# Kernel optimization log

Hardware: AMD Instinct MI355X
Metric: run time of the kernel (lower is better)

The kernel has to match this reference:

```python
import jax, jax.numpy as jnp
import numpy as np

EPS = 1e-5  # BatchNorm eps (torch default)


def point_sample(feat, points):
    """Bilinear sample feat [B,C,Hf,Wf] at points [B,K,2] (x,y in [0,1]),
    matching F.grid_sample(2*p-1, mode='bilinear', padding_mode='zeros',
    align_corners=False)."""
    B, C, Hf, Wf = feat.shape
    x = points[..., 0] * Wf - 0.5  # [B,K] pixel coords
    y = points[..., 1] * Hf - 0.5
    x0f = jnp.floor(x); y0f = jnp.floor(y)
    wx = (x - x0f)[:, None, :]  # [B,1,K]
    wy = (y - y0f)[:, None, :]
    x0 = x0f.astype(jnp.int32); y0 = y0f.astype(jnp.int32)
    flat = feat.reshape(B, C, Hf * Wf)

    def gather(xi, yi):
        valid = ((xi >= 0) & (xi < Wf) & (yi >= 0) & (yi < Hf))[:, None, :]
        lin = jnp.clip(yi, 0, Hf - 1) * Wf + jnp.clip(xi, 0, Wf - 1)  # [B,K]
        idx = jnp.broadcast_to(lin[:, None, :], (B, C, lin.shape[1]))
        return jnp.take_along_axis(flat, idx, axis=2) * valid

    v00 = gather(x0, y0)
    v10 = gather(x0 + 1, y0)
    v01 = gather(x0, y0 + 1)
    v11 = gather(x0 + 1, y0 + 1)
    return (v00 * (1 - wx) * (1 - wy) + v10 * wx * (1 - wy)
            + v01 * (1 - wx) * wy + v11 * wx * wy)


def bn(x, g, b, m, v):
    # eval-mode BatchNorm1d over channel dim of [B,C,K]
    scale = (g / jnp.sqrt(v + EPS))[None, :, None]
    return (x - m[None, :, None]) * scale + b[None, :, None]


def setup_inputs() -> dict:
    key = jax.random.key(0)
    ks = jax.random.split(key, 20)
    B, H, W = 8, 512, 512
    Cf = 256
    d = {
        'uncertainty_map': jax.random.normal(ks[0], (B, 1, H, W), jnp.float32),
        'prev_mask': jax.random.uniform(ks[1], (B, 1, H, W), jnp.float32),
        'enc_f': jax.random.normal(ks[2], (B, Cf, 128, 128), jnp.float32),
        'w1': jax.random.normal(ks[3], (256, Cf + 1), jnp.float32) * 0.05,
        'b1': jax.random.normal(ks[4], (256,), jnp.float32) * 0.05,
        'g1': jnp.ones((256,), jnp.float32),
        'be1': jnp.zeros((256,), jnp.float32),
        'm1': jax.random.normal(ks[5], (256,), jnp.float32) * 0.1,
        'v1': jax.random.uniform(ks[6], (256,), jnp.float32) + 0.5,
        'w2': jax.random.normal(ks[7], (256, 256), jnp.float32) * 0.05,
        'b2': jax.random.normal(ks[8], (256,), jnp.float32) * 0.05,
        'g2': jnp.ones((256,), jnp.float32),
        'be2': jnp.zeros((256,), jnp.float32),
        'm2': jax.random.normal(ks[9], (256,), jnp.float32) * 0.1,
        'v2': jax.random.uniform(ks[10], (256,), jnp.float32) + 0.5,
        'w3': jax.random.normal(ks[11], (1, 256), jnp.float32) * 0.05,
        'b3': jax.random.normal(ks[12], (1,), jnp.float32) * 0.05,
    }
    return d


def reference(uncertainty_map, prev_mask, enc_f,
              w1, b1, g1, be1, m1, v1,
              w2, b2, g2, be2, m2, v2,
              w3, b3):
    B, C, H, W = prev_mask.shape
    K = H * W // 10
    # K least-uncertain points (topk largest=False)
    _, idx = jax.lax.top_k(-uncertainty_map.reshape(B, -1), K)  # [B,K] int32
    col = (idx % W).astype(jnp.float32)
    row = (idx // W).astype(jnp.float32)
    points = jnp.stack([(col + 0.5) / W, (row + 0.5) / H], axis=-1)  # [B,K,2]

    coarse = point_sample(prev_mask, points)  # [B,1,K]
    fine = point_sample(enc_f, points)        # [B,Cf,K]
    h = jnp.concatenate([coarse, fine], axis=1)  # [B,Cf+1,K]

    h = jax.nn.relu(bn(jnp.einsum('oc,bck->bok', w1, h) + b1[None, :, None], g1, be1, m1, v1))
    h = jax.nn.relu(bn(jnp.einsum('oc,bck->bok', w2, h) + b2[None, :, None], g2, be2, m2, v2))
    refined = jax.nn.sigmoid(jnp.einsum('oc,bck->bok', w3, h) + b3[None, :, None])  # [B,1,K]

    flat = prev_mask.reshape(B, C, H * W)
    bi = jnp.arange(B)[:, None, None]
    ci = jnp.arange(C)[None, :, None]
    out = flat.at[bi, ci, idx[:, None, :]].set(jnp.broadcast_to(refined, (B, C, K)))
    return out.reshape(B, C, H, W)
```

## Files before the change

### kernel.cpp

```cpp
#include <hip/hip_runtime.h>
#include <hip/hip_bf16.h>

#define HW_IMG 262144
#define KSEL   26214
#define NB     8
#define CF     256
#define LDW1   288
#define LDACT  296

typedef short    short8 __attribute__((ext_vector_type(8)));
typedef float    f32x4  __attribute__((ext_vector_type(4)));
typedef unsigned u32x2  __attribute__((ext_vector_type(2)));
typedef unsigned short u16x4 __attribute__((ext_vector_type(4)));

__device__ __forceinline__ unsigned f2key(float f){
    unsigned u = __builtin_bit_cast(unsigned, f);
    return (u & 0x80000000u) ? ~u : (u | 0x80000000u);
}
__device__ __forceinline__ unsigned short f2bf(float f){
    unsigned u = __builtin_bit_cast(unsigned, f);
    u = u + 0x7FFFu + ((u >> 16) & 1u);
    return (unsigned short)(u >> 16);
}
__device__ __forceinline__ float bf2f(unsigned short s){
    unsigned u = ((unsigned)s) << 16;
    return __builtin_bit_cast(float, u);
}

__global__ __launch_bounds__(256) void k_prep(
    const float* __restrict__ w1, const float* __restrict__ w2,
    const float* __restrict__ b1, const float* __restrict__ g1, const float* __restrict__ be1,
    const float* __restrict__ m1, const float* __restrict__ v1,
    const float* __restrict__ b2, const float* __restrict__ g2, const float* __restrict__ be2,
    const float* __restrict__ m2, const float* __restrict__ v2,
    unsigned short* __restrict__ w1p, unsigned short* __restrict__ w2p,
    float* __restrict__ c1, float* __restrict__ c2)
{
    int tid = blockIdx.x * 256 + threadIdx.x;
    if (tid < 256 * LDW1) {
        int o = tid / LDW1, k = tid % LDW1;
        float scale = g1[o] * rsqrtf(v1[o] + 1e-5f);
        float val = 0.f;
        if (k < 256) val = w1[o * 257 + k + 1];
        else if (k == 256) val = w1[o * 257];
        w1p[tid] = f2bf(val * scale);
        if (k == 0) c1[o] = (b1[o] - m1[o]) * scale + be1[o];
    } else {
        int t2 = tid - 256 * LDW1;
        if (t2 < 65536) {
            int o = t2 >> 8;
            float scale = g2[o] * rsqrtf(v2[o] + 1e-5f);
            w2p[t2] = f2bf(w2[t2] * scale);
            if ((t2 & 255) == 0) c2[o] = (b2[o] - m2[o]) * scale + be2[o];
        }
    }
}

__global__ __launch_bounds__(256) void k_transpose(
    const float* __restrict__ enc, unsigned short* __restrict__ encT)
{
    __shared__ __align__(16) unsigned short tile[64][72];
    int b = blockIdx.z;
    int pixbase = blockIdx.x * 64;
    int chbase  = blockIdx.y * 64;
    int t = threadIdx.x;
    int pix = t & 63, cg = t >> 6;
    const float* src = enc + (size_t)b * CF * 16384;
#pragma unroll
    for (int i = 0; i < 16; i++) {
        int c = chbase + cg * 16 + i;
        tile[pix][cg * 16 + i] = f2bf(src[(size_t)c * 16384 + pixbase + pix]);
    }
    __syncthreads();
    unsigned short* dst = encT + (size_t)b * 16384 * CF;
#pragma unroll
    for (int pass = 0; pass < 4; pass++) {
        int pl = pass * 16 + (t >> 4);
        int c4 = (t & 15) * 4;
        *(u16x4*)(dst + (size_t)(pixbase + pl) * CF + chbase + c4) = *(const u16x4*)&tile[pl][c4];
    }
}


__global__ __launch_bounds__(256) void k_histA(const float* __restrict__ unc, unsigned* __restrict__ hist)
{
    __shared__ unsigned lh[4][4096];
    int b = blockIdx.y, t = threadIdx.x;
    int wv = t >> 6;
    for (int i = t; i < 4 * 4096; i += 256) ((unsigned*)lh)[i] = 0;
    __syncthreads();
    const float4* src = (const float4*)(unc + (size_t)b * HW_IMG + blockIdx.x * 4096);
    unsigned* mine = lh[wv];
#pragma unroll
    for (int j = 0; j < 4; j++) {
        float4 v = src[j * 256 + t];
        atomicAdd(&mine[f2key(v.x) >> 20], 1u);
        atomicAdd(&mine[f2key(v.y) >> 20], 1u);
        atomicAdd(&mine[f2key(v.z) >> 20], 1u);
        atomicAdd(&mine[f2key(v.w) >> 20], 1u);
    }
    __syncthreads();
    unsigned* gh = hist + (size_t)b * 4096;
    for (int i = t; i < 4096; i += 256) {
        unsigned c = lh[0][i] + lh[1][i] + lh[2][i] + lh[3][i];
        if (c) atomicAdd(&gh[i], c);
    }
}

__global__ __launch_bounds__(256) void k_histB(const float* __restrict__ unc,
    const unsigned* __restrict__ meta, unsigned* __restrict__ hist)
{
    __shared__ unsigned lh[4096];
    int b = blockIdx.y, t = threadIdx.x;
    unsigned binA = meta[b * 8 + 0];
    for (int i = t; i < 4096; i += 256) lh[i] = 0;
    __syncthreads();
    const float4* src = (const float4*)(unc + (size_t)b * HW_IMG + blockIdx.x * 4096);
#pragma unroll
    for (int j = 0; j < 4; j++) {
        float4 v = src[j * 256 + t];
        unsigned k;
        k = f2key(v.x); if ((k >> 20) == binA) atomicAdd(&lh[(k >> 8) & 0xFFFu], 1u);
        k = f2key(v.y); if ((k >> 20) == binA) atomicAdd(&lh[(k >> 8) & 0xFFFu], 1u);
        k = f2key(v.z); if ((k >> 20) == binA) atomicAdd(&lh[(k >> 8) & 0xFFFu], 1u);
        k = f2key(v.w); if ((k >> 20) == binA) atomicAdd(&lh[(k >> 8) & 0xFFFu], 1u);
    }
    __syncthreads();
    unsigned* gh = hist + (size_t)b * 4096;
    for (int i = t; i < 4096; i += 256) { unsigned c = lh[i]; if (c) atomicAdd(&gh[i], c); }
}

__global__ __launch_bounds__(256) void k_histC(const float* __restrict__ unc,
    const unsigned* __restrict__ meta, unsigned* __restrict__ hist)
{
    __shared__ unsigned lh[256];
    int b = blockIdx.y, t = threadIdx.x;
    unsigned pre24 = (meta[b * 8 + 0] << 12) | meta[b * 8 + 2];
    lh[t] = 0;
    __syncthreads();
    const float4* src = (const float4*)(unc + (size_t)b * HW_IMG + blockIdx.x * 4096);
#pragma unroll
    for (int j = 0; j < 4; j++) {
        float4 v = src[j * 256 + t];
        unsigned k;
        k = f2key(v.x); if ((k >> 8) == pre24) atomicAdd(&lh[k & 0xFFu], 1u);
        k = f2key(v.y); if ((k >> 8) == pre24) atomicAdd(&lh[k & 0xFFu], 1u);
        k = f2key(v.z); if ((k >> 8) == pre24) atomicAdd(&lh[k & 0xFFu], 1u);
        k = f2key(v.w); if ((k >> 8) == pre24) atomicAdd(&lh[k & 0xFFu], 1u);
    }
    __syncthreads();
    unsigned* gh = hist + (size_t)b * 4096;
    unsigned c = lh[t];
    if (c) atomicAdd(&gh[t], c);
}

__global__ __launch_bounds__(256) void k_find(const unsigned* __restrict__ hist,
    unsigned* __restrict__ meta, int per, int stage)
{
    int b = blockIdx.x, t = threadIdx.x;
    const unsigned* h = hist + (size_t)b * 4096;
    unsigned base = (stage == 0) ? 0u : meta[b * 8 + 2 * stage - 1];
    __shared__ unsigned seg[256], pref[256];
    unsigned s = 0;
    for (int i = 0; i < per; i++) s += h[t * per + i];
    seg[t] = s;
    __syncthreads();
    if (t == 0) { unsigned c = base; for (int i = 0; i < 256; i++) { pref[i] = c; c += seg[i]; } }
    __syncthreads();
    if (pref[t] < KSEL && KSEL <= pref[t] + seg[t]) {
        unsigned c = pref[t];
        for (int i = 0; i < per; i++) {
            unsigned cnt = h[t * per + i];
            if (c + cnt >= KSEL) {
                unsigned bin = (unsigned)(t * per + i);
                meta[b * 8 + 2 * stage] = bin;
                meta[b * 8 + 2 * stage + 1] = c;
                if (stage == 2)
                    meta[b * 8 + 6] = (meta[b * 8 + 0] << 20) | (meta[b * 8 + 2] << 8) | bin;
                break;
            }
            c += cnt;
        }
    }
}

__global__ __launch_bounds__(256) void k_count(const float* __restrict__ unc,
    const unsigned* __restrict__ meta, unsigned* __restrict__ cntL, unsigned* __restrict__ cntE)
{
    int b = blockIdx.y, blk = blockIdx.x, t = threadIdx.x;
    unsigned pivot = meta[b * 8 + 6];
    const float4* src = (const float4*)(unc + (size_t)b * HW_IMG + blk * 1024);
    float4 v = src[t];
    unsigned k0 = f2key(v.x), k1 = f2key(v.y), k2 = f2key(v.z), k3 = f2key(v.w);
    unsigned cl = (k0 < pivot) + (k1 < pivot) + (k2 < pivot) + (k3 < pivot);
    unsigned ce = (k0 == pivot) + (k1 == pivot) + (k2 == pivot) + (k3 == pivot);
    __shared__ unsigned rl[256], re[256];
    rl[t] = cl; re[t] = ce; __syncthreads();
    for (int s = 128; s > 0; s >>= 1) { if (t < s) { rl[t] += rl[t + s]; re[t] += re[t + s]; } __syncthreads(); }
    if (t == 0) { cntL[b * 256 + blk] = rl[0]; cntE[b * 256 + blk] = re[0]; }
}

__global__ void k_scan(const unsigned* __restrict__ cntL, const unsigned* __restrict__ cntE,
                       unsigned* __restrict__ offL, unsigned* __restrict__ offE)
{
    int b = blockIdx.x;
    if (threadIdx.x == 0) {
        unsigned c = 0;
        for (int i = 0; i < 256; i++) { offL[b * 256 + i] = c; c += cntL[b * 256 + i]; }
        c = 0;
        for (int i = 0; i < 256; i++) { offE[b * 256 + i] = c; c += cntE[b * 256 + i]; }
    }
}

__global__ __launch_bounds__(256) void k_emit(const float* __restrict__ unc,
    const unsigned* __restrict__ meta, const unsigned* __restrict__ offL,
    const unsigned* __restrict__ offE, unsigned* __restrict__ sel)
{
    int b = blockIdx.y, blk = blockIdx.x, t = threadIdx.x;
    unsigned pivot = meta[b * 8 + 6], cless = meta[b * 8 + 5], r = KSEL - cless;
    int base = blk * 1024 + t * 4;
    const float4* src = (const float4*)(unc + (size_t)b * HW_IMG + blk * 1024);
    float4 v = src[t];
    unsigned key[4] = { f2key(v.x), f2key(v.y), f2key(v.z), f2key(v.w) };
    unsigned cl = 0, ce = 0;
#pragma unroll
    for (int j = 0; j < 4; j++) { cl += (key[j] < pivot); ce += (key[j] == pivot); }
    __shared__ unsigned sL[256], sE[256];
    sL[t] = cl; sE[t] = ce; __syncthreads();
    for (int off = 1; off < 256; off <<= 1) {
        unsigned aL = (t >= off) ? sL[t - off] : 0u;
        unsigned aE = (t >= off) ? sE[t - off] : 0u;
        __syncthreads();
        sL[t] += aL; sE[t] += aE;
        __syncthreads();
    }
    unsigned posL = offL[b * 256 + blk] + sL[t] - cl;
    unsigned posE = offE[b * 256 + blk] + sE[t] - ce;
    unsigned* sb = sel + (size_t)b * KSEL;
#pragma unroll
    for (int j = 0; j < 4; j++) {
        if (key[j] < pivot) { sb[posL++] = (unsigned)(base + j); }
        else if (key[j] == pivot) { if (posE < r) sb[cless + posE] = (unsigned)(base + j); posE++; }
    }
}

__global__ __launch_bounds__(256, 2) void k_main(
    const unsigned* __restrict__ sel, const float* __restrict__ prev,
    const unsigned short* __restrict__ encT,
    const unsigned short* __restrict__ w1p, const unsigned short* __restrict__ w2p,
    const float* __restrict__ c1, const float* __restrict__ c2,
    const float* __restrict__ w3, const float* __restrict__ b3,
    float* __restrict__ out)
{
    __shared__ __align__(16) unsigned short act[64][LDACT];
    __shared__ unsigned sIdx[64];
    __shared__ float sPart[4][64];

    int b = blockIdx.y;
    int pbase = blockIdx.x * 64;
    int npts = KSEL - pbase; if (npts > 64) npts = 64;
    int t = threadIdx.x;

    if (t < 64) {
        unsigned id = (t < npts) ? sel[(size_t)b * KSEL + pbase + t] : 0u;
        sIdx[t] = id;
        act[t][256] = f2bf(prev[(size_t)b * HW_IMG + id]);
#pragma unroll
        for (int k = 257; k < LDW1; k++) act[t][k] = 0;
    }
    __syncthreads();

    {
        int wv = t >> 6, l = t & 63;
        int g = l >> 2, sub = l & 3;
        int p = wv * 16 + g;
        unsigned id = sIdx[p];
        int col = id & 511, row = (int)(id >> 9);
        float xf = (col - 1.5f) * 0.25f;
        float yf = (row - 1.5f) * 0.25f;
        float x0f = floorf(xf), y0f = floorf(yf);
        int x0 = (int)x0f, y0 = (int)y0f;
        float wx = xf - x0f, wy = yf - y0f;
        float wxa = (x0 >= 0) ? (1.f - wx) : 0.f;
        float wxb = (x0 <= 126) ? wx : 0.f;
        float wya = (y0 >= 0) ? (1.f - wy) : 0.f;
        float wyb = (y0 <= 126) ? wy : 0.f;
        int xc0 = x0 < 0 ? 0 : x0;
        int xc1 = (x0 + 1 > 127) ? 127 : x0 + 1;
        int yc0 = y0 < 0 ? 0 : y0;
        int yc1 = (y0 + 1 > 127) ? 127 : y0 + 1;
        float w00 = wxa * wya, w10 = wxb * wya, w01 = wxa * wyb, w11 = wxb * wyb;
        const unsigned short* bb = encT + (size_t)b * 16384 * CF + sub * 64;
        const unsigned short* p00 = bb + (size_t)(yc0 * 128 + xc0) * CF;
        const unsigned short* p10 = bb + (size_t)(yc0 * 128 + xc1) * CF;
        const unsigned short* p01 = bb + (size_t)(yc1 * 128 + xc0) * CF;
        const unsigned short* p11 = bb + (size_t)(yc1 * 128 + xc1) * CF;
#pragma unroll 2
        for (int ch = 0; ch < 8; ch++) {
            short8 va = *(const short8*)(p00 + ch * 8);
            short8 vb = *(const short8*)(p10 + ch * 8);
            short8 vc = *(const short8*)(p01 + ch * 8);
            short8 vd = *(const short8*)(p11 + ch * 8);
            short8 rr;
#pragma unroll
            for (int j = 0; j < 8; j++) {
                float f = w00 * bf2f((unsigned short)va[j]) + w10 * bf2f((unsigned short)vb[j])
                        + w01 * bf2f((unsigned short)vc[j]) + w11 * bf2f((unsigned short)vd[j]);
                rr[j] = (short)f2bf(f);
            }
            *(short8*)&act[p][sub * 64 + ch * 8] = rr;
        }
    }
    __syncthreads();

    int wv = t >> 6, l = t & 63;
    int lr = l & 15, lk = l >> 4;
    f32x4 acc[4][4];
#pragma unroll
    for (int m = 0; m < 4; m++)
#pragma unroll
        for (int n = 0; n < 4; n++) acc[m][n] = (f32x4){0.f, 0.f, 0.f, 0.f};

#pragma unroll
    for (int kk = 0; kk < 9; kk++) {
        int k0 = kk * 32 + lk * 8;
        short8 afr[4], bfr[4];
#pragma unroll
        for (int m = 0; m < 4; m++)
            afr[m] = *(const short8*)(w1p + (size_t)(wv * 64 + m * 16 + lr) * LDW1 + k0);
#pragma unroll
        for (int n = 0; n < 4; n++)
            bfr[n] = *(const short8*)&act[n * 16 + lr][k0];
#pragma unroll
        for (int m = 0; m < 4; m++)
#pragma unroll
            for (int n = 0; n < 4; n++)
                acc[m][n] = __builtin_amdgcn_mfma_f32_16x16x32_bf16(afr[m], bfr[n], acc[m][n], 0, 0, 0);
    }
    __syncthreads();

#pragma unroll
    for (int m = 0; m < 4; m++) {
        int chb = wv * 64 + m * 16 + lk * 4;
        float c0 = c1[chb], cA = c1[chb + 1], cB = c1[chb + 2], cC = c1[chb + 3];
#pragma unroll
        for (int n = 0; n < 4; n++) {
            int p = n * 16 + lr;
            float v0 = fmaxf(acc[m][n][0] + c0, 0.f);
            float v1 = fmaxf(acc[m][n][1] + cA, 0.f);
            float v2 = fmaxf(acc[m][n][2] + cB, 0.f);
            float v3 = fmaxf(acc[m][n][3] + cC, 0.f);
            u32x2 pk;
            pk[0] = (unsigned)f2bf(v0) | ((unsigned)f2bf(v1) << 16);
            pk[1] = (unsigned)f2bf(v2) | ((unsigned)f2bf(v3) << 16);
            *(u32x2*)&act[p][chb] = pk;
        }
    }
    __syncthreads();

#pragma unroll
    for (int m = 0; m < 4; m++)
#pragma unroll
        for (int n = 0; n < 4; n++) acc[m][n] = (f32x4){0.f, 0.f, 0.f, 0.f};
#pragma unroll
    for (int kk = 0; kk < 8; kk++) {
        int k0 = kk * 32 + lk * 8;
        short8 afr[4], bfr[4];
#pragma unroll
        for (int m = 0; m < 4; m++)
            afr[m] = *(const short8*)(w2p + (size_t)(wv * 64 + m * 16 + lr) * 256 + k0);
#pragma unroll
        for (int n = 0; n < 4; n++)
            bfr[n] = *(const short8*)&act[n * 16 + lr][k0];
#pragma unroll
        for (int m = 0; m < 4; m++)
#pragma unroll
            for (int n = 0; n < 4; n++)
                acc[m][n] = __builtin_amdgcn_mfma_f32_16x16x32_bf16(afr[m], bfr[n], acc[m][n], 0, 0, 0);
    }

    float part[4] = {0.f, 0.f, 0.f, 0.f};
#pragma unroll
    for (int m = 0; m < 4; m++) {
        int chb = wv * 64 + m * 16 + lk * 4;
#pragma unroll
        for (int r = 0; r < 4; r++) {
            float wr = w3[chb + r];
            float cr = c2[chb + r];
#pragma unroll
            for (int n = 0; n < 4; n++)
                part[n] += wr * fmaxf(acc[m][n][r] + cr, 0.f);
        }
    }
#pragma unroll
    for (int n = 0; n < 4; n++) {
        part[n] += __shfl_xor(part[n], 16);
        part[n] += __shfl_xor(part[n], 32);
    }
    if (lk == 0) {
#pragma unroll
        for (int n = 0; n < 4; n++) sPart[wv][n * 16 + lr] = part[n];
    }
    __syncthreads();
    if (t < 64) {
        float tot = sPart[0][t] + sPart[1][t] + sPart[2][t] + sPart[3][t] + b3[0];
        float refined = 1.f / (1.f + __expf(-tot));
        if (t < npts) out[(size_t)b * HW_IMG + sIdx[t]] = refined;
    }
}

extern "C" void kernel_launch(void* const* d_in, const int* in_sizes, int n_in,
                              void* d_out, int out_size, void* d_ws, size_t ws_size,
                              hipStream_t stream)
{
    (void)in_sizes; (void)n_in; (void)out_size; (void)ws_size;
    const float* unc  = (const float*)d_in[0];
    const float* prev = (const float*)d_in[1];
    const float* enc  = (const float*)d_in[2];
    const float* w1   = (const float*)d_in[3];
    const float* b1   = (const float*)d_in[4];
    const float* g1   = (const float*)d_in[5];
    const float* be1  = (const float*)d_in[6];
    const float* m1   = (const float*)d_in[7];
    const float* v1   = (const float*)d_in[8];
    const float* w2   = (const float*)d_in[9];
    const float* b2   = (const float*)d_in[10];
    const float* g2   = (const float*)d_in[11];
    const float* be2  = (const float*)d_in[12];
    const float* m2   = (const float*)d_in[13];
    const float* v2   = (const float*)d_in[14];
    const float* w3   = (const float*)d_in[15];
    const float* b3   = (const float*)d_in[16];
    float* out = (float*)d_out;

    char* ws = (char*)d_ws;
    size_t off = 0;
    auto alloc = [&](size_t bytes) { size_t o = off; off += (bytes + 255) & ~(size_t)255; return o; };
    size_t o_encT = alloc((size_t)NB * 16384 * CF * 2);
    size_t o_w1p  = alloc((size_t)256 * LDW1 * 2);
    size_t o_w2p  = alloc((size_t)256 * 256 * 2);
    size_t o_c1   = alloc(256 * 4);
    size_t o_c2   = alloc(256 * 4);
    size_t o_hist = alloc((size_t)3 * NB * 4096 * 4);
    size_t o_meta = alloc(NB * 8 * 4);
    size_t o_cntL = alloc(NB * 256 * 4);
    size_t o_cntE = alloc(NB * 256 * 4);
    size_t o_offL = alloc(NB * 256 * 4);
    size_t o_offE = alloc(NB * 256 * 4);
    size_t o_sel  = alloc((size_t)NB * KSEL * 4);

    unsigned short* encT = (unsigned short*)(ws + o_encT);
    unsigned short* w1p  = (unsigned short*)(ws + o_w1p);
    unsigned short* w2p  = (unsigned short*)(ws + o_w2p);
    float* c1p = (float*)(ws + o_c1);
    float* c2p = (float*)(ws + o_c2);
    unsigned* histA = (unsigned*)(ws + o_hist);
    unsigned* histB = histA + (size_t)NB * 4096;
    unsigned* histC = histB + (size_t)NB * 4096;
    unsigned* meta  = (unsigned*)(ws + o_meta);
    unsigned* cntL  = (unsigned*)(ws + o_cntL);
    unsigned* cntE  = (unsigned*)(ws + o_cntE);
    unsigned* offL  = (unsigned*)(ws + o_offL);
    unsigned* offE  = (unsigned*)(ws + o_offE);
    unsigned* sel   = (unsigned*)(ws + o_sel);

    hipMemsetAsync(ws + o_hist, 0, (size_t)3 * NB * 4096 * 4, stream);
    hipMemcpyAsync(d_out, (const void*)prev, (size_t)NB * HW_IMG * 4, hipMemcpyDeviceToDevice, stream);

    k_prep<<<544, 256, 0, stream>>>(w1, w2, b1, g1, be1, m1, v1, b2, g2, be2, m2, v2,
                                    w1p, w2p, c1p, c2p);
    k_transpose<<<dim3(256, 4, NB), 256, 0, stream>>>(enc, encT);

    k_histA<<<dim3(64, NB), 256, 0, stream>>>(unc, histA);
    k_find <<<NB, 256, 0, stream>>>(histA, meta, 16, 0);
    k_histB<<<dim3(64, NB), 256, 0, stream>>>(unc, meta, histB);
    k_find <<<NB, 256, 0, stream>>>(histB, meta, 16, 1);
    k_histC<<<dim3(64, NB), 256, 0, stream>>>(unc, meta, histC);
    k_find <<<NB, 256, 0, stream>>>(histC, meta, 1, 2);
    k_count<<<dim3(256, NB), 256, 0, stream>>>(unc, meta, cntL, cntE);
    k_scan <<<NB, 64, 0, stream>>>(cntL, cntE, offL, offE);
    k_emit <<<dim3(256, NB), 256, 0, stream>>>(unc, meta, offL, offE, sel);

    k_main<<<dim3((KSEL + 63) / 64, NB), 256, 0, stream>>>(sel, prev, encT, w1p, w2p,
                                                           c1p, c2p, w3, b3, out);
}
```

Baseline: 244.8 us.

## Fuse find/scan stages into histogram kernels via last-block pattern and swizzle activation LDS

Removes the separate k_find and k_scan launches by having the last finishing block per batch (found with an atomic done counter) run the threshold search or a parallel prefix scan. This cuts kernel launches and serial single-thread scans. The main kernel also gets an XOR-swizzled activation layout in shared memory to reduce bank conflicts, a higher occupancy target, a flattened batch-interleaved grid, deeper unrolling of the gather loop, and no shared-memory index staging. The risks are extra atomics and fences, and possible register spills under the tighter launch bounds.

```diff
diff --git a/kernel.cpp b/kernel.cpp
--- a/kernel.cpp
+++ b/kernel.cpp
@@ -7,6 +7,9 @@
 #define CF     256
 #define LDW1   288
 #define LDACT  296
+#define NBLK_MAIN 410
+
+#define ACOL(c) ((c) ^ ((((c) >> 6) & 3) << 4))
 
 typedef short    short8 __attribute__((ext_vector_type(8)));
 typedef float    f32x4  __attribute__((ext_vector_type(4)));
@@ -82,90 +85,18 @@
 }
 
 
-__global__ __launch_bounds__(256) void k_histA(const float* __restrict__ unc, unsigned* __restrict__ hist)
-{
-    __shared__ unsigned lh[4][4096];
-    int b = blockIdx.y, t = threadIdx.x;
-    int wv = t >> 6;
-    for (int i = t; i < 4 * 4096; i += 256) ((unsigned*)lh)[i] = 0;
-    __syncthreads();
-    const float4* src = (const float4*)(unc + (size_t)b * HW_IMG + blockIdx.x * 4096);
-    unsigned* mine = lh[wv];
-#pragma unroll
-    for (int j = 0; j < 4; j++) {
-        float4 v = src[j * 256 + t];
-        atomicAdd(&mine[f2key(v.x) >> 20], 1u);
-        atomicAdd(&mine[f2key(v.y) >> 20], 1u);
-        atomicAdd(&mine[f2key(v.z) >> 20], 1u);
-        atomicAdd(&mine[f2key(v.w) >> 20], 1u);
-    }
-    __syncthreads();
-    unsigned* gh = hist + (size_t)b * 4096;
-    for (int i = t; i < 4096; i += 256) {
-        unsigned c = lh[0][i] + lh[1][i] + lh[2][i] + lh[3][i];
-        if (c) atomicAdd(&gh[i], c);
-    }
-}
-
-__global__ __launch_bounds__(256) void k_histB(const float* __restrict__ unc,
-    const unsigned* __restrict__ meta, unsigned* __restrict__ hist)
-{
-    __shared__ unsigned lh[4096];
-    int b = blockIdx.y, t = threadIdx.x;
-    unsigned binA = meta[b * 8 + 0];
-    for (int i = t; i < 4096; i += 256) lh[i] = 0;
-    __syncthreads();
-    const float4* src = (const float4*)(unc + (size_t)b * HW_IMG + blockIdx.x * 4096);
-#pragma unroll
-    for (int j = 0; j < 4; j++) {
-        float4 v = src[j * 256 + t];
-        unsigned k;
-        k = f2key(v.x); if ((k >> 20) == binA) atomicAdd(&lh[(k >> 8) & 0xFFFu], 1u);
-        k = f2key(v.y); if ((k >> 20) == binA) atomicAdd(&lh[(k >> 8) & 0xFFFu], 1u);
-        k = f2key(v.z); if ((k >> 20) == binA) atomicAdd(&lh[(k >> 8) & 0xFFFu], 1u);
-        k = f2key(v.w); if ((k >> 20) == binA) atomicAdd(&lh[(k >> 8) & 0xFFFu], 1u);
-    }
-    __syncthreads();
-    unsigned* gh = hist + (size_t)b * 4096;
-    for (int i = t; i < 4096; i += 256) { unsigned c = lh[i]; if (c) atomicAdd(&gh[i], c); }
-}
-
-__global__ __launch_bounds__(256) void k_histC(const float* __restrict__ unc,
-    const unsigned* __restrict__ meta, unsigned* __restrict__ hist)
-{
-    __shared__ unsigned lh[256];
-    int b = blockIdx.y, t = threadIdx.x;
-    unsigned pre24 = (meta[b * 8 + 0] << 12) | meta[b * 8 + 2];
-    lh[t] = 0;
-    __syncthreads();
-    const float4* src = (const float4*)(unc + (size_t)b * HW_IMG + blockIdx.x * 4096);
-#pragma unroll
-    for (int j = 0; j < 4; j++) {
-        float4 v = src[j * 256 + t];
-        unsigned k;
-        k = f2key(v.x); if ((k >> 8) == pre24) atomicAdd(&lh[k & 0xFFu], 1u);
-        k = f2key(v.y); if ((k >> 8) == pre24) atomicAdd(&lh[k & 0xFFu], 1u);
-        k = f2key(v.z); if ((k >> 8) == pre24) atomicAdd(&lh[k & 0xFFu], 1u);
-        k = f2key(v.w); if ((k >> 8) == pre24) atomicAdd(&lh[k & 0xFFu], 1u);
-    }
-    __syncthreads();
-    unsigned* gh = hist + (size_t)b * 4096;
-    unsigned c = lh[t];
-    if (c) atomicAdd(&gh[t], c);
-}
-
-__global__ __launch_bounds__(256) void k_find(const unsigned* __restrict__ hist,
-    unsigned* __restrict__ meta, int per, int stage)
-{
-    int b = blockIdx.x, t = threadIdx.x;
-    const unsigned* h = hist + (size_t)b * 4096;
-    unsigned base = (stage == 0) ? 0u : meta[b * 8 + 2 * stage - 1];
+__device__ __forceinline__ void find_stage(const unsigned* __restrict__ h,
+    unsigned* __restrict__ meta, int b, int per, int stage, int t)
+{
     __shared__ unsigned seg[256], pref[256];
     unsigned s = 0;
     for (int i = 0; i < per; i++) s += h[t * per + i];
     seg[t] = s;
     __syncthreads();
-    if (t == 0) { unsigned c = base; for (int i = 0; i < 256; i++) { pref[i] = c; c += seg[i]; } }
+    if (t == 0) {
+        unsigned c = (stage == 0) ? 0u : meta[b * 8 + 2 * stage - 1];
+        for (int i = 0; i < 256; i++) { pref[i] = c; c += seg[i]; }
+    }
     __syncthreads();
     if (pref[t] < KSEL && KSEL <= pref[t] + seg[t]) {
         unsigned c = pref[t];
@@ -184,8 +115,98 @@
     }
 }
 
+__device__ __forceinline__ bool last_block(unsigned* done, int b, int nblk, int t)
+{
+    __shared__ unsigned sT;
+    __threadfence();
+    __syncthreads();
+    if (t == 0) sT = atomicAdd(&done[b], 1u);
+    __syncthreads();
+    if (sT == (unsigned)(nblk - 1)) { __threadfence(); return true; }
+    return false;
+}
+
+__global__ __launch_bounds__(256) void k_histA(const float* __restrict__ unc,
+    unsigned* __restrict__ hist, unsigned* __restrict__ meta, unsigned* __restrict__ done)
+{
+    __shared__ unsigned lh[4][4096];
+    int b = blockIdx.y, t = threadIdx.x;
+    int wv = t >> 6;
+    for (int i = t; i < 4 * 4096; i += 256) ((unsigned*)lh)[i] = 0;
+    __syncthreads();
+    const float4* src = (const float4*)(unc + (size_t)b * HW_IMG + blockIdx.x * 4096);
+    unsigned* mine = lh[wv];
+#pragma unroll
+    for (int j = 0; j < 4; j++) {
+        float4 v = src[j * 256 + t];
+        atomicAdd(&mine[f2key(v.x) >> 20], 1u);
+        atomicAdd(&mine[f2key(v.y) >> 20], 1u);
+        atomicAdd(&mine[f2key(v.z) >> 20], 1u);
+        atomicAdd(&mine[f2key(v.w) >> 20], 1u);
+    }
+    __syncthreads();
+    unsigned* gh = hist + (size_t)b * 4096;
+    for (int i = t; i < 4096; i += 256) {
+        unsigned c = lh[0][i] + lh[1][i] + lh[2][i] + lh[3][i];
+        if (c) atomicAdd(&gh[i], c);
+    }
+    if (last_block(done, b, gridDim.x, t)) find_stage(gh, meta, b, 16, 0, t);
+}
+
+__global__ __launch_bounds__(256) void k_histB(const float* __restrict__ unc,
+    const unsigned* __restrict__ metaIn, unsigned* __restrict__ hist,
+    unsigned* __restrict__ meta, unsigned* __restrict__ done)
+{
+    __shared__ unsigned lh[4096];
+    int b = blockIdx.y, t = threadIdx.x;
+    unsigned binA = metaIn[b * 8 + 0];
+    for (int i = t; i < 4096; i += 256) lh[i] = 0;
+    __syncthreads();
+    const float4* src = (const float4*)(unc + (size_t)b * HW_IMG + blockIdx.x * 4096);
+#pragma unroll
+    for (int j = 0; j < 4; j++) {
+        float4 v = src[j * 256 + t];
+        unsigned k;
+        k = f2key(v.x); if ((k >> 20) == binA) atomicAdd(&lh[(k >> 8) & 0xFFFu], 1u);
+        k = f2key(v.y); if ((k >> 20) == binA) atomicAdd(&lh[(k >> 8) & 0xFFFu], 1u);
+        k = f2key(v.z); if ((k >> 20) == binA) atomicAdd(&lh[(k >> 8) & 0xFFFu], 1u);
+        k = f2key(v.w); if ((k >> 20) == binA) atomicAdd(&lh[(k >> 8) & 0xFFFu], 1u);
+    }
+    __syncthreads();
+    unsigned* gh = hist + (size_t)b * 4096;
+    for (int i = t; i < 4096; i += 256) { unsigned c = lh[i]; if (c) atomicAdd(&gh[i], c); }
+    if (last_block(done, b, gridDim.x, t)) find_stage(gh, meta, b, 16, 1, t);
+}
+
+__global__ __launch_bounds__(256) void k_histC(const float* __restrict__ unc,
+    const unsigned* __restrict__ metaIn, unsigned* __restrict__ hist,
+    unsigned* __restrict__ meta, unsigned* __restrict__ done)
+{
+    __shared__ unsigned lh[256];
+    int b = blockIdx.y, t = threadIdx.x;
+    unsigned pre24 = (metaIn[b * 8 + 0] << 12) | metaIn[b * 8 + 2];
+    lh[t] = 0;
+    __syncthreads();
+    const float4* src = (const float4*)(unc + (size_t)b * HW_IMG + blockIdx.x * 4096);
+#pragma unroll
+    for (int j = 0; j < 4; j++) {
+        float4 v = src[j * 256 + t];
+        unsigned k;
+        k = f2key(v.x); if ((k >> 8) == pre24) atomicAdd(&lh[k & 0xFFu], 1u);
+        k = f2key(v.y); if ((k >> 8) == pre24) atomicAdd(&lh[k & 0xFFu], 1u);
+        k = f2key(v.z); if ((k >> 8) == pre24) atomicAdd(&lh[k & 0xFFu], 1u);
+        k = f2key(v.w); if ((k >> 8) == pre24) atomicAdd(&lh[k & 0xFFu], 1u);
+    }
+    __syncthreads();
+    unsigned* gh = hist + (size_t)b * 4096;
+    unsigned c = lh[t];
+    if (c) atomicAdd(&gh[t], c);
+    if (last_block(done, b, gridDim.x, t)) find_stage(gh, meta, b, 1, 2, t);
+}
+
 __global__ __launch_bounds__(256) void k_count(const float* __restrict__ unc,
-    const unsigned* __restrict__ meta, unsigned* __restrict__ cntL, unsigned* __restrict__ cntE)
+    const unsigned* __restrict__ meta, unsigned* __restrict__ cntL, unsigned* __restrict__ cntE,
+    unsigned* __restrict__ offL, unsigned* __restrict__ offE, unsigned* __restrict__ done)
 {
     int b = blockIdx.y, blk = blockIdx.x, t = threadIdx.x;
     unsigned pivot = meta[b * 8 + 6];
@@ -198,17 +219,19 @@
     rl[t] = cl; re[t] = ce; __syncthreads();
     for (int s = 128; s > 0; s >>= 1) { if (t < s) { rl[t] += rl[t + s]; re[t] += re[t + s]; } __syncthreads(); }
     if (t == 0) { cntL[b * 256 + blk] = rl[0]; cntE[b * 256 + blk] = re[0]; }
-}
-
-__global__ void k_scan(const unsigned* __restrict__ cntL, const unsigned* __restrict__ cntE,
-                       unsigned* __restrict__ offL, unsigned* __restrict__ offE)
-{
-    int b = blockIdx.x;
-    if (threadIdx.x == 0) {
-        unsigned c = 0;
-        for (int i = 0; i < 256; i++) { offL[b * 256 + i] = c; c += cntL[b * 256 + i]; }
-        c = 0;
-        for (int i = 0; i < 256; i++) { offE[b * 256 + i] = c; c += cntE[b * 256 + i]; }
+    if (last_block(done, b, gridDim.x, t)) {
+        unsigned vL = cntL[b * 256 + t], vE = cntE[b * 256 + t];
+        rl[t] = vL; re[t] = vE;
+        __syncthreads();
+        for (int off = 1; off < 256; off <<= 1) {
+            unsigned aL = (t >= off) ? rl[t - off] : 0u;
+            unsigned aE = (t >= off) ? re[t - off] : 0u;
+            __syncthreads();
+            rl[t] += aL; re[t] += aE;
+            __syncthreads();
+        }
+        offL[b * 256 + t] = rl[t] - vL;
+        offE[b * 256 + t] = re[t] - vE;
     }
 }
 
@@ -244,7 +267,7 @@
     }
 }
 
-__global__ __launch_bounds__(256, 2) void k_main(
+__global__ __launch_bounds__(256, 3) void k_main(
     const unsigned* __restrict__ sel, const float* __restrict__ prev,
     const unsigned short* __restrict__ encT,
     const unsigned short* __restrict__ w1p, const unsigned short* __restrict__ w2p,
@@ -253,28 +276,21 @@
     float* __restrict__ out)
 {
     __shared__ __align__(16) unsigned short act[64][LDACT];
-    __shared__ unsigned sIdx[64];
     __shared__ float sPart[4][64];
 
-    int b = blockIdx.y;
-    int pbase = blockIdx.x * 64;
+    int wg = blockIdx.x;
+    int b  = wg & 7;
+    int pbase = (wg >> 3) * 64;
     int npts = KSEL - pbase; if (npts > 64) npts = 64;
     int t = threadIdx.x;
-
-    if (t < 64) {
-        unsigned id = (t < npts) ? sel[(size_t)b * KSEL + pbase + t] : 0u;
-        sIdx[t] = id;
-        act[t][256] = f2bf(prev[(size_t)b * HW_IMG + id]);
-#pragma unroll
-        for (int k = 257; k < LDW1; k++) act[t][k] = 0;
-    }
-    __syncthreads();
+    const unsigned* selb = sel + (size_t)b * KSEL;
 
     {
-        int wv = t >> 6, l = t & 63;
-        int g = l >> 2, sub = l & 3;
-        int p = wv * 16 + g;
-        unsigned id = sIdx[p];
+        int wv2 = t >> 6, l2 = t & 63;
+        int g = l2 >> 2, sub = l2 & 3;
+        int p = wv2 * 16 + g;
+        int gi = pbase + p; if (gi >= KSEL) gi = KSEL - 1;
+        unsigned id = selb[gi];
         int col = id & 511, row = (int)(id >> 9);
         float xf = (col - 1.5f) * 0.25f;
         float yf = (row - 1.5f) * 0.25f;
@@ -295,7 +311,7 @@
         const unsigned short* p10 = bb + (size_t)(yc0 * 128 + xc1) * CF;
         const unsigned short* p01 = bb + (size_t)(yc1 * 128 + xc0) * CF;
         const unsigned short* p11 = bb + (size_t)(yc1 * 128 + xc1) * CF;
-#pragma unroll 2
+#pragma unroll 4
         for (int ch = 0; ch < 8; ch++) {
             short8 va = *(const short8*)(p00 + ch * 8);
             short8 vb = *(const short8*)(p10 + ch * 8);
@@ -308,8 +324,19 @@
                         + w01 * bf2f((unsigned short)vc[j]) + w11 * bf2f((unsigned short)vd[j]);
                 rr[j] = (short)f2bf(f);
             }
-            *(short8*)&act[p][sub * 64 + ch * 8] = rr;
+            *(short8*)&act[p][ACOL(sub * 64 + ch * 8)] = rr;
         }
+    }
+    if (t < 64) {
+        int gi = pbase + t; if (gi >= KSEL) gi = KSEL - 1;
+        unsigned id = selb[gi];
+        float cv = prev[(size_t)b * HW_IMG + id];
+        short8 z = {0,0,0,0,0,0,0,0};
+        short8 c8 = z; c8[0] = (short)f2bf(cv);
+        *(short8*)&act[t][256] = c8;
+        *(short8*)&act[t][264] = z;
+        *(short8*)&act[t][272] = z;
+        *(short8*)&act[t][280] = z;
     }
     __syncthreads();
 
@@ -324,13 +351,14 @@
 #pragma unroll
     for (int kk = 0; kk < 9; kk++) {
         int k0 = kk * 32 + lk * 8;
+        int k0s = ACOL(k0);
         short8 afr[4], bfr[4];
 #pragma unroll
         for (int m = 0; m < 4; m++)
             afr[m] = *(const short8*)(w1p + (size_t)(wv * 64 + m * 16 + lr) * LDW1 + k0);
 #pragma unroll
         for (int n = 0; n < 4; n++)
-            bfr[n] = *(const short8*)&act[n * 16 + lr][k0];
+            bfr[n] = *(const short8*)&act[n * 16 + lr][k0s];
 #pragma unroll
         for (int m = 0; m < 4; m++)
 #pragma unroll
@@ -342,6 +370,7 @@
 #pragma unroll
     for (int m = 0; m < 4; m++) {
         int chb = wv * 64 + m * 16 + lk * 4;
+        int chbs = ACOL(chb);
         float c0 = c1[chb], cA = c1[chb + 1], cB = c1[chb + 2], cC = c1[chb + 3];
 #pragma unroll
         for (int n = 0; n < 4; n++) {
@@ -353,7 +382,7 @@
             u32x2 pk;
             pk[0] = (unsigned)f2bf(v0) | ((unsigned)f2bf(v1) << 16);
             pk[1] = (unsigned)f2bf(v2) | ((unsigned)f2bf(v3) << 16);
-            *(u32x2*)&act[p][chb] = pk;
+            *(u32x2*)&act[p][chbs] = pk;
         }
     }
     __syncthreads();
@@ -365,13 +394,14 @@
 #pragma unroll
     for (int kk = 0; kk < 8; kk++) {
         int k0 = kk * 32 + lk * 8;
+        int k0s = ACOL(k0);
         short8 afr[4], bfr[4];
 #pragma unroll
         for (int m = 0; m < 4; m++)
             afr[m] = *(const short8*)(w2p + (size_t)(wv * 64 + m * 16 + lr) * 256 + k0);
 #pragma unroll
         for (int n = 0; n < 4; n++)
-            bfr[n] = *(const short8*)&act[n * 16 + lr][k0];
+            bfr[n] = *(const short8*)&act[n * 16 + lr][k0s];
 #pragma unroll
         for (int m = 0; m < 4; m++)
 #pragma unroll
@@ -402,10 +432,11 @@
         for (int n = 0; n < 4; n++) sPart[wv][n * 16 + lr] = part[n];
     }
     __syncthreads();
-    if (t < 64) {
+    if (t < 64 && t < npts) {
         float tot = sPart[0][t] + sPart[1][t] + sPart[2][t] + sPart[3][t] + b3[0];
         float refined = 1.f / (1.f + __expf(-tot));
-        if (t < npts) out[(size_t)b * HW_IMG + sIdx[t]] = refined;
+        unsigned id = selb[pbase + t];
+        out[(size_t)b * HW_IMG + id] = refined;
     }
 }
 
@@ -441,7 +472,8 @@
     size_t o_w2p  = alloc((size_t)256 * 256 * 2);
     size_t o_c1   = alloc(256 * 4);
     size_t o_c2   = alloc(256 * 4);
-    size_t o_hist = alloc((size_t)3 * NB * 4096 * 4);
+    size_t histBytes = (size_t)3 * NB * 4096 * 4;
+    size_t o_hist = alloc(histBytes + 4 * NB * 4);
     size_t o_meta = alloc(NB * 8 * 4);
     size_t o_cntL = alloc(NB * 256 * 4);
     size_t o_cntE = alloc(NB * 256 * 4);
@@ -457,6 +489,10 @@
     unsigned* histA = (unsigned*)(ws + o_hist);
     unsigned* histB = histA + (size_t)NB * 4096;
     unsigned* histC = histB + (size_t)NB * 4096;
+    unsigned* doneA = histC + (size_t)NB * 4096;
+    unsigned* doneB = doneA + NB;
+    unsigned* doneC = doneB + NB;
+    unsigned* doneN = doneC + NB;
     unsigned* meta  = (unsigned*)(ws + o_meta);
     unsigned* cntL  = (unsigned*)(ws + o_cntL);
     unsigned* cntE  = (unsigned*)(ws + o_cntE);
@@ -464,23 +500,19 @@
     unsigned* offE  = (unsigned*)(ws + o_offE);
     unsigned* sel   = (unsigned*)(ws + o_sel);
 
-    hipMemsetAsync(ws + o_hist, 0, (size_t)3 * NB * 4096 * 4, stream);
+    hipMemsetAsync(ws + o_hist, 0, histBytes + 4 * NB * 4, stream);
     hipMemcpyAsync(d_out, (const void*)prev, (size_t)NB * HW_IMG * 4, hipMemcpyDeviceToDevice, stream);
 
     k_prep<<<544, 256, 0, stream>>>(w1, w2, b1, g1, be1, m1, v1, b2, g2, be2, m2, v2,
                                     w1p, w2p, c1p, c2p);
     k_transpose<<<dim3(256, 4, NB), 256, 0, stream>>>(enc, encT);
 
-    k_histA<<<dim3(64, NB), 256, 0, stream>>>(unc, histA);
-    k_find <<<NB, 256, 0, stream>>>(histA, meta, 16, 0);
-    k_histB<<<dim3(64, NB), 256, 0, stream>>>(unc, meta, histB);
-    k_find <<<NB, 256, 0, stream>>>(histB, meta, 16, 1);
-    k_histC<<<dim3(64, NB), 256, 0, stream>>>(unc, meta, histC);
-    k_find <<<NB, 256, 0, stream>>>(histC, meta, 1, 2);
-    k_count<<<dim3(256, NB), 256, 0, stream>>>(unc, meta, cntL, cntE);
-    k_scan <<<NB, 64, 0, stream>>>(cntL, cntE, offL, offE);
+    k_histA<<<dim3(64, NB), 256, 0, stream>>>(unc, histA, meta, doneA);
+    k_histB<<<dim3(64, NB), 256, 0, stream>>>(unc, meta, histB, meta, doneB);
+    k_histC<<<dim3(64, NB), 256, 0, stream>>>(unc, meta, histC, meta, doneC);
+    k_count<<<dim3(256, NB), 256, 0, stream>>>(unc, meta, cntL, cntE, offL, offE, doneN);
     k_emit <<<dim3(256, NB), 256, 0, stream>>>(unc, meta, offL, offE, sel);
 
-    k_main<<<dim3((KSEL + 63) / 64, NB), 256, 0, stream>>>(sel, prev, encT, w1p, w2p,
-                                                           c1p, c2p, w3, b3, out);
-}
+    k_main<<<NBLK_MAIN * NB, 256, 0, stream>>>(sel, prev, encT, w1p, w2p,
+                                               c1p, c2p, w3, b3, out);
+}
```

After: 455.6 us. 1.86x slower.
